# Kernel tuning notes

Hardware: AMD Instinct MI355X
Metric: run time of the kernel (lower is better)

Reference implementation:

```python
import jax, jax.numpy as jnp
import numpy as np

B, M, N, C = 1, 128, 256, 256
MID, OUT_C = 32, 128
LN_EPS = 1e-5
NORM_EPS = 1e-3


def setup_inputs() -> dict:
    key = jax.random.key(0)
    ks = jax.random.split(key, 9)
    act = jax.random.normal(ks[0], (B, M, N, C), dtype=jnp.float32)
    mask = (jax.random.uniform(ks[1], (B, M, N)) < 0.9).astype(jnp.float32)
    s_in = 1.0 / np.sqrt(C)
    s_mid = 1.0 / np.sqrt(MID * MID)
    return {
        "act": act,
        "mask": mask,
        "ln_g": jnp.ones((C,), jnp.float32),
        "ln_b": jnp.zeros((C,), jnp.float32),
        "lw": jax.random.normal(ks[2], (MID, C), jnp.float32) * s_in,
        "lb": jnp.zeros((MID,), jnp.float32),
        "rw": jax.random.normal(ks[3], (MID, C), jnp.float32) * s_in,
        "rb": jnp.zeros((MID,), jnp.float32),
        "ow": jax.random.normal(ks[4], (OUT_C, MID * MID), jnp.float32) * s_mid,
        "ob": jnp.zeros((OUT_C,), jnp.float32),
    }


def reference(act, mask, ln_g, ln_b, lw, lb, rw, rb, ow, ob):
    # LayerNorm over channel dim
    mu = jnp.mean(act, axis=-1, keepdims=True)
    var = jnp.mean(jnp.square(act - mu), axis=-1, keepdims=True)
    x = (act - mu) * jax.lax.rsqrt(var + LN_EPS) * ln_g + ln_b  # [b,m,i,c]

    m = mask[..., None]  # [b,m,i,1]
    left = m * (jnp.einsum('bmic,xc->bmix', x, lw) + lb)   # [b,m,i,mid]
    right = m * (jnp.einsum('bmic,yc->bmiy', x, rw) + rb)  # [b,m,i,mid]

    # outer product mean over MSA dim m -> [b,i,j,x,y]
    x2d = jnp.einsum('bmix,bmjy->bijxy', left, right)
    x2d = x2d.reshape(x2d.shape[:3] + (MID * MID,))
    out = jnp.einsum('bijk,ok->bijo', x2d, ow) + ob  # [b,i,j,out_c]

    norm = jnp.einsum('bmi,bmj->bij', mask, mask)[..., None]
    return out / (norm + NORM_EPS)
```

## Files before the change

kernel.cpp:

```cpp
#include <hip/hip_runtime.h>
#include <hip/hip_bf16.h>

typedef __bf16 bf16x8 __attribute__((ext_vector_type(8)));
typedef __bf16 bf16x4 __attribute__((ext_vector_type(4)));
typedef float  f32x4  __attribute__((ext_vector_type(4)));
typedef float  f32x16 __attribute__((ext_vector_type(16)));

#define MDIM 128
#define NDIM 256
#define CDIM 256
#define MIDC 32
#define OUTC 128

#define LSX_RS 1156
#define LSX_YS 36
#define LSX_BYTES (32 * LSX_RS * 2)

__global__ __launch_bounds__(256) void prep_kernel(
    const float* __restrict__ mask,
    const float* __restrict__ lw, const float* __restrict__ lb,
    const float* __restrict__ rw, const float* __restrict__ rb,
    const float* __restrict__ ow,
    __bf16* __restrict__ wb, float* __restrict__ cbias,
    __bf16* __restrict__ owb_f, float* __restrict__ norm_inv)
{
    int b = blockIdx.x, t = threadIdx.x;
    if (b < 256) {
        float s = 0.f;
        #pragma unroll 8
        for (int m = 0; m < MDIM; ++m)
            s += mask[m*NDIM + b] * mask[m*NDIM + t];
        norm_inv[b*NDIM + t] = 1.0f / (s + 1e-3f);
    } else if (b < 320) {
        int e0 = (b - 256)*2048 + t*8;
        #pragma unroll
        for (int jj = 0; jj < 8; ++jj) {
            int e = e0 + jj;
            int lane = (e >> 3) & 63;
            int s = (e >> 9) & 63;
            int ot = e >> 15;
            int o = ot*32 + (lane & 31);
            int x = (s & 1)*16 + (lane >> 5)*8 + jj;
            int y = s >> 1;
            owb_f[e] = (__bf16)ow[o*1024 + x*32 + y];
        }
    } else {
        int e0 = (b - 320)*2048 + t*8;
        #pragma unroll
        for (int j = 0; j < 8; ++j) {
            int e = e0 + j;
            int row = e >> 8, c = e & 255;
            wb[e] = (__bf16)(row < MIDC ? lw[row*CDIM + c] : rw[(row - MIDC)*CDIM + c]);
        }
        if (b == 320 && t < 64) cbias[t] = (t < MIDC) ? lb[t] : rb[t - MIDC];
    }
}

__global__ __launch_bounds__(256) void ln_proj_kernel(
    const float* __restrict__ act, const float* __restrict__ mask,
    const float* __restrict__ ln_g, const float* __restrict__ ln_b,
    const __bf16* __restrict__ wb, const float* __restrict__ cbias,
    __bf16* __restrict__ left_f, __bf16* __restrict__ right_f)
{
    __shared__ __bf16 xls[64][264];
    __shared__ __bf16 T[64][72];
    int t = threadIdx.x, lane = t & 63, w = t >> 6;
    int quad = lane >> 4, l16 = lane & 15;
    int b  = blockIdx.x;
    int m0 = blockIdx.y * 64;

    float4 gv = *(const float4*)(ln_g + lane*4);
    float4 bv = *(const float4*)(ln_b + lane*4);
    const float inv_c = 1.0f / 256.0f;

    #pragma unroll 4
    for (int s = 0; s < 16; ++s) {
        int m = m0 + w*16 + s;
        float4 v = *(const float4*)(act + ((size_t)m*NDIM + b)*CDIM + lane*4);
        float sum = v.x + v.y + v.z + v.w;
        float ssq = v.x*v.x + v.y*v.y + v.z*v.z + v.w*v.w;
        #pragma unroll
        for (int d = 1; d < 64; d <<= 1) {
            sum += __shfl_xor(sum, d);
            ssq += __shfl_xor(ssq, d);
        }
        float mu   = sum * inv_c;
        float var  = ssq * inv_c - mu*mu;
        float rstd = rsqrtf(var + 1e-5f);
        bf16x4 o;
        o.x = (__bf16)((v.x - mu)*rstd*gv.x + bv.x);
        o.y = (__bf16)((v.y - mu)*rstd*gv.y + bv.y);
        o.z = (__bf16)((v.z - mu)*rstd*gv.z + bv.z);
        o.w = (__bf16)((v.w - mu)*rstd*gv.w + bv.w);
        *(bf16x4*)&xls[w*16 + s][lane*4] = o;
    }

    f32x4 acc[4] = {};
    const __bf16* arow = &xls[w*16 + l16][0];
    #pragma unroll
    for (int k0 = 0; k0 < 256; k0 += 32) {
        bf16x8 a = *(const bf16x8*)(arow + k0 + quad*8);
        #pragma unroll
        for (int tt = 0; tt < 4; ++tt) {
            bf16x8 bb = *(const bf16x8*)(wb + (size_t)(tt*16 + l16)*CDIM + k0 + quad*8);
            acc[tt] = __builtin_amdgcn_mfma_f32_16x16x32_bf16(a, bb, acc[tt], 0, 0, 0);
        }
    }

    #pragma unroll
    for (int rg = 0; rg < 4; ++rg) {
        int ml = w*16 + quad*4 + rg;
        float mval = mask[(size_t)(m0 + ml)*NDIM + b];
        #pragma unroll
        for (int tt = 0; tt < 4; ++tt) {
            int o = tt*16 + l16;
            T[o][ml] = (__bf16)(mval * (acc[tt][rg] + cbias[o]));
        }
    }
    __syncthreads();

    {
        int fl16  = t & 15;
        int r     = t >> 4;
        int q     = r & 3;
        int k0loc = (r >> 2) & 1;
        int half  = (r >> 3) & 1;
        int tile  = b*2 + half;
        int k0    = (m0 >> 5) + k0loc;
        size_t dstoff = (((size_t)tile*4 + k0)*64 + q*16 + fl16)*8;
        #pragma unroll
        for (int side = 0; side < 2; ++side) {
            int o = side*32 + half*16 + fl16;
            bf16x8 d = *(const bf16x8*)&T[o][k0loc*32 + q*8];
            __bf16* dst = side ? right_f : left_f;
            *(bf16x8*)(dst + dstoff) = d;
        }
    }
}

__global__ __launch_bounds__(512, 4) void outer_kernel(
    const __bf16* __restrict__ left_f, const __bf16* __restrict__ right_f,
    const __bf16* __restrict__ owb_f, const float* __restrict__ ob,
    const float* __restrict__ norm_inv, float* __restrict__ out)
{
    extern __shared__ __bf16 lsX[];
    int t = threadIdx.x, lane = t & 63, w = t >> 6;
    int quad = lane >> 4, l16 = lane & 15;
    int l31 = lane & 31, half = lane >> 5;

    int id = blockIdx.x;
    int xcd = id & 7, p = id >> 3;
    int bi = xcd*8 + (p & 7);
    int bj = p >> 3;

    int wr = w & 1, wc = w >> 1;
    const __bf16* Af = left_f  + ((size_t)(bi*8  + wr*4)*4)*512 + lane*8;
    const __bf16* Bf = right_f + ((size_t)(bj*16 + wc*4)*4)*512 + lane*8;

    f32x4 acc1[4][4] = {};
    #pragma unroll
    for (int kk = 0; kk < 4; ++kk) {
        bf16x8 af[4], bg[4];
        #pragma unroll
        for (int tr = 0; tr < 4; ++tr) af[tr] = *(const bf16x8*)(Af + tr*2048 + kk*512);
        #pragma unroll
        for (int tc = 0; tc < 4; ++tc) bg[tc] = *(const bf16x8*)(Bf + tc*2048 + kk*512);
        #pragma unroll
        for (int tr = 0; tr < 4; ++tr)
            #pragma unroll
            for (int tc = 0; tc < 4; ++tc)
                acc1[tr][tc] = __builtin_amdgcn_mfma_f32_16x16x32_bf16(af[tr], bg[tc], acc1[tr][tc], 0, 0, 0);
    }

    int ot = w & 3, kh = w >> 2;
    const __bf16* Ob = owb_f + ((size_t)(ot*64 + kh*32)*64 + lane)*8;
    bf16x8 bbuf0 = *(const bf16x8*)(Ob);
    bf16x8 bbuf1 = *(const bf16x8*)(Ob + 512);

    #pragma unroll
    for (int tr = 0; tr < 4; ++tr) {
        int il = wr*2 + (tr >> 1);
        int x0 = (tr & 1)*16 + quad*4;
        #pragma unroll
        for (int tc = 0; tc < 4; ++tc) {
            int jl = wc*2 + (tc >> 1);
            int y  = (tc & 1)*16 + l16;
            bf16x4 pk;
            pk.x = (__bf16)acc1[tr][tc][0];
            pk.y = (__bf16)acc1[tr][tc][1];
            pk.z = (__bf16)acc1[tr][tc][2];
            pk.w = (__bf16)acc1[tr][tc][3];
            *(bf16x4*)(lsX + (size_t)(il*8 + jl)*LSX_RS + y*LSX_YS + x0) = pk;
        }
    }
    __syncthreads();

    f32x16 acc2 = {};
    const __bf16* Xb = lsX + (size_t)l31*LSX_RS + half*8;
    #pragma unroll 4
    for (int ss = 0; ss < 32; ++ss) {
        int s = kh*32 + ss;
        bf16x8 bb = bbuf0;
        bbuf0 = bbuf1;
        if (ss + 2 < 32) bbuf1 = *(const bf16x8*)(Ob + (ss + 2)*512);
        int xoff = (s >> 1)*LSX_YS + (s & 1)*16;
        const __bf16* ap = Xb + xoff;
        bf16x4 lo = *(const bf16x4*)(ap);
        bf16x4 hi = *(const bf16x4*)(ap + 4);
        bf16x8 a  = __builtin_shufflevector(lo, hi, 0, 1, 2, 3, 4, 5, 6, 7);
        acc2 = __builtin_amdgcn_mfma_f32_32x32x16_bf16(a, bb, acc2, 0, 0, 0);
    }
    __syncthreads();

    float* scr = (float*)lsX;
    if (kh == 1) {
        int base = ot*1024;
        #pragma unroll
        for (int r = 0; r < 16; ++r) {
            int row = (r & 3) + 8*(r >> 2) + 4*half;
            scr[base + row*32 + l31] = acc2[r];
        }
    }
    __syncthreads();

    if (kh == 0) {
        int o = ot*32 + l31;
        float obv = ob[o];
        #pragma unroll
        for (int r = 0; r < 16; ++r) {
            int row = (r & 3) + 8*(r >> 2) + 4*half;
            float v = acc2[r] + scr[ot*1024 + row*32 + l31];
            int i = bi*4 + (row >> 3), j = bj*8 + (row & 7);
            out[((size_t)(i*NDIM + j))*OUTC + o] = (v + obv) * norm_inv[i*NDIM + j];
        }
    }
}

extern "C" void kernel_launch(void* const* d_in, const int* in_sizes, int n_in,
                              void* d_out, int out_size, void* d_ws, size_t ws_size,
                              hipStream_t stream) {
    const float* act  = (const float*)d_in[0];
    const float* mask = (const float*)d_in[1];
    const float* ln_g = (const float*)d_in[2];
    const float* ln_b = (const float*)d_in[3];
    const float* lw   = (const float*)d_in[4];
    const float* lb   = (const float*)d_in[5];
    const float* rw   = (const float*)d_in[6];
    const float* rb   = (const float*)d_in[7];
    const float* ow   = (const float*)d_in[8];
    const float* ob   = (const float*)d_in[9];
    float* out = (float*)d_out;

    unsigned char* ws = (unsigned char*)d_ws;
    __bf16* left_f   = (__bf16*)(ws + 0);
    __bf16* right_f  = (__bf16*)(ws + (2u<<20));
    __bf16* owb_f    = (__bf16*)(ws + (4u<<20));
    float*  norm_inv = (float*) (ws + (4u<<20) + (256u<<10));
    __bf16* wb       = (__bf16*)(ws + (4u<<20) + (512u<<10));
    float*  cbias    = (float*) (ws + (4u<<20) + (544u<<10));

    hipFuncSetAttribute((const void*)outer_kernel,
                        hipFuncAttributeMaxDynamicSharedMemorySize, LSX_BYTES);

    prep_kernel<<<328, 256, 0, stream>>>(mask, lw, lb, rw, rb, ow,
                                         wb, cbias, owb_f, norm_inv);
    ln_proj_kernel<<<dim3(256, 2), 256, 0, stream>>>(act, mask, ln_g, ln_b,
                                                     wb, cbias, left_f, right_f);
    outer_kernel<<<2048, 512, LSX_BYTES, stream>>>(left_f, right_f, owb_f, ob,
                                                   norm_inv, out);
}
```

Measured before the change: 161.2 us.

## Stage left tile in LDS, double-buffer right loads, deepen output-weight prefetch

The block's left-factor tile is now staged into shared memory once by all threads, so the eight waves no longer each fetch their A fragments from global memory. Right-factor fragments are double-buffered across the k loop. Output-weight fragments are prefetched eight steps ahead instead of two. The second GEMM splits into two independent accumulators to break the MFMA dependency chain. These changes add register pressure and an extra barrier, which may hurt occupancy under the 512-thread, 4-block launch bound.

```diff
diff --git a/kernel.cpp b/kernel.cpp
--- a/kernel.cpp
+++ b/kernel.cpp
@@ -153,29 +153,49 @@
     int bi = xcd*8 + (p & 7);
     int bj = p >> 3;
 
+    {
+        uint4* ls4 = (uint4*)lsX;
+        const uint4* gA4 = (const uint4*)(left_f + (size_t)bi*16384);
+        #pragma unroll
+        for (int r = 0; r < 4; ++r) ls4[r*512 + t] = gA4[r*512 + t];
+    }
+    __syncthreads();
+
     int wr = w & 1, wc = w >> 1;
-    const __bf16* Af = left_f  + ((size_t)(bi*8  + wr*4)*4)*512 + lane*8;
-    const __bf16* Bf = right_f + ((size_t)(bj*16 + wc*4)*4)*512 + lane*8;
+    const __bf16* lsA = lsX + (size_t)(wr*4)*2048 + lane*8;
+    const __bf16* Bf  = right_f + ((size_t)(bj*16 + wc*4)*4)*512 + lane*8;
+
+    bf16x8 bg[2][4];
+    #pragma unroll
+    for (int tc = 0; tc < 4; ++tc) bg[0][tc] = *(const bf16x8*)(Bf + tc*2048);
 
     f32x4 acc1[4][4] = {};
     #pragma unroll
     for (int kk = 0; kk < 4; ++kk) {
-        bf16x8 af[4], bg[4];
-        #pragma unroll
-        for (int tr = 0; tr < 4; ++tr) af[tr] = *(const bf16x8*)(Af + tr*2048 + kk*512);
-        #pragma unroll
-        for (int tc = 0; tc < 4; ++tc) bg[tc] = *(const bf16x8*)(Bf + tc*2048 + kk*512);
+        if (kk < 3) {
+            #pragma unroll
+            for (int tc = 0; tc < 4; ++tc)
+                bg[(kk + 1) & 1][tc] = *(const bf16x8*)(Bf + tc*2048 + (kk + 1)*512);
+        }
+        bf16x8 af[4];
+        #pragma unroll
+        for (int tr = 0; tr < 4; ++tr)
+            af[tr] = *(const bf16x8*)(lsA + tr*2048 + kk*512);
         #pragma unroll
         for (int tr = 0; tr < 4; ++tr)
             #pragma unroll
             for (int tc = 0; tc < 4; ++tc)
-                acc1[tr][tc] = __builtin_amdgcn_mfma_f32_16x16x32_bf16(af[tr], bg[tc], acc1[tr][tc], 0, 0, 0);
+                acc1[tr][tc] = __builtin_amdgcn_mfma_f32_16x16x32_bf16(
+                    af[tr], bg[kk & 1][tc], acc1[tr][tc], 0, 0, 0);
     }
 
     int ot = w & 3, kh = w >> 2;
     const __bf16* Ob = owb_f + ((size_t)(ot*64 + kh*32)*64 + lane)*8;
-    bf16x8 bbuf0 = *(const bf16x8*)(Ob);
-    bf16x8 bbuf1 = *(const bf16x8*)(Ob + 512);
+    bf16x8 rb[8];
+    #pragma unroll
+    for (int r = 0; r < 8; ++r) rb[r] = *(const bf16x8*)(Ob + r*512);
+
+    __syncthreads();
 
     #pragma unroll
     for (int tr = 0; tr < 4; ++tr) {
@@ -195,21 +215,32 @@
     }
     __syncthreads();
 
-    f32x16 acc2 = {};
+    f32x16 acc2a = {}, acc2b = {};
     const __bf16* Xb = lsX + (size_t)l31*LSX_RS + half*8;
-    #pragma unroll 4
-    for (int ss = 0; ss < 32; ++ss) {
-        int s = kh*32 + ss;
-        bf16x8 bb = bbuf0;
-        bbuf0 = bbuf1;
-        if (ss + 2 < 32) bbuf1 = *(const bf16x8*)(Ob + (ss + 2)*512);
-        int xoff = (s >> 1)*LSX_YS + (s & 1)*16;
-        const __bf16* ap = Xb + xoff;
-        bf16x4 lo = *(const bf16x4*)(ap);
-        bf16x4 hi = *(const bf16x4*)(ap + 4);
-        bf16x8 a  = __builtin_shufflevector(lo, hi, 0, 1, 2, 3, 4, 5, 6, 7);
-        acc2 = __builtin_amdgcn_mfma_f32_32x32x16_bf16(a, bb, acc2, 0, 0, 0);
-    }
+    #pragma unroll
+    for (int ss = 0; ss < 32; ss += 2) {
+        {
+            int s = kh*32 + ss;
+            int xoff = (s >> 1)*LSX_YS + (s & 1)*16;
+            const __bf16* ap = Xb + xoff;
+            bf16x4 lo = *(const bf16x4*)(ap);
+            bf16x4 hi = *(const bf16x4*)(ap + 4);
+            bf16x8 a  = __builtin_shufflevector(lo, hi, 0, 1, 2, 3, 4, 5, 6, 7);
+            acc2a = __builtin_amdgcn_mfma_f32_32x32x16_bf16(a, rb[ss & 7], acc2a, 0, 0, 0);
+        }
+        if (ss + 8 < 32) rb[ss & 7] = *(const bf16x8*)(Ob + (ss + 8)*512);
+        {
+            int s = kh*32 + ss + 1;
+            int xoff = (s >> 1)*LSX_YS + (s & 1)*16;
+            const __bf16* ap = Xb + xoff;
+            bf16x4 lo = *(const bf16x4*)(ap);
+            bf16x4 hi = *(const bf16x4*)(ap + 4);
+            bf16x8 a  = __builtin_shufflevector(lo, hi, 0, 1, 2, 3, 4, 5, 6, 7);
+            acc2b = __builtin_amdgcn_mfma_f32_32x32x16_bf16(a, rb[(ss + 1) & 7], acc2b, 0, 0, 0);
+        }
+        if (ss + 9 < 32) rb[(ss + 1) & 7] = *(const bf16x8*)(Ob + (ss + 9)*512);
+    }
+    f32x16 acc2 = acc2a + acc2b;
     __syncthreads();
 
     float* scr = (float*)lsX;
```

New measurement: 151.8 us. 1.06x faster.
